# Optimization experiments

Measured on AMD Instinct MI355X. Metric: run time of the kernel, lower is better.

Reference implementation:

```python
import jax, jax.numpy as jnp
import numpy as np

D_MODEL = 1024
NUM_HEADS = 16
D_K = D_MODEL // NUM_HEADS


def setup_inputs() -> dict:
    key = jax.random.key(0)
    ks = jax.random.split(key, 11)
    s = 1.0 / np.sqrt(D_MODEL)
    return {
        "Q": jax.random.normal(ks[0], (2, 2048, D_MODEL), jnp.float32),
        "K": jax.random.normal(ks[1], (2, 2048, D_MODEL), jnp.float32),
        "V": jax.random.normal(ks[2], (2, 2048, D_MODEL), jnp.float32),
        "W_Q": jax.random.uniform(ks[3], (D_MODEL, D_MODEL), jnp.float32, -s, s),
        "b_Q": jax.random.uniform(ks[4], (D_MODEL,), jnp.float32, -s, s),
        "W_K": jax.random.uniform(ks[5], (D_K, D_MODEL), jnp.float32, -s, s),
        "b_K": jax.random.uniform(ks[6], (D_K,), jnp.float32, -s, s),
        "W_V": jax.random.uniform(ks[7], (D_K, D_MODEL), jnp.float32, -s, s),
        "b_V": jax.random.uniform(ks[8], (D_K,), jnp.float32, -s, s),
        "W_O": jax.random.uniform(ks[9], (D_MODEL, D_MODEL), jnp.float32, -s, s),
        "b_O": jax.random.uniform(ks[10], (D_MODEL,), jnp.float32, -s, s),
    }


def reference(Q, K, V, W_Q, b_Q, W_K, b_K, W_V, b_V, W_O, b_O):
    B, S, _ = Q.shape
    # Q projection -> [B, H, S, d_k]
    q = (Q @ W_Q.T + b_Q).reshape(B, S, NUM_HEADS, D_K).transpose(0, 2, 1, 3)
    # shared single-head K/V -> [B, S, d_k] (broadcast across heads)
    k = K @ W_K.T + b_K
    v = V @ W_V.T + b_V
    scale = 1.0 / jnp.sqrt(jnp.asarray(D_K, q.dtype))
    scores = jnp.einsum('bhqd,bkd->bhqk', q, k) * scale  # [B,H,S,S]
    attn = jax.nn.softmax(scores, axis=-1)
    out = jnp.einsum('bhqk,bkd->bhqd', attn, v)  # [B,H,S,d_k]
    out = out.transpose(0, 2, 1, 3).reshape(B, S, D_MODEL)
    return out @ W_O.T + b_O
```

## Files before the change

kernel.cpp:

```cpp
#include <hip/hip_runtime.h>
#include <hip/hip_bf16.h>
#include <math.h>

#define D_MODEL 1024
#define NUM_HEADS 16
#define DK 64
#define BATCH 2
#define SEQ 2048
#define MROWS (BATCH * SEQ)

#define QSCALE (0.125f * 1.4426950408889634f)

typedef __attribute__((ext_vector_type(8))) short bf16x8;
typedef __attribute__((ext_vector_type(4))) float f32x4;

static __device__ __forceinline__ short f2bf(float f) {
    __hip_bfloat16 h = __float2bfloat16(f);
    union { __hip_bfloat16 h; short s; } c; c.h = h; return c.s;
}

static __device__ __forceinline__ unsigned pkbf2(float a, float b) {
    __hip_bfloat162 h = __float22bfloat162_rn(make_float2(a, b));
    union { __hip_bfloat162 h; unsigned u; } c; c.h = h; return c.u;
}

static __device__ __forceinline__ void gload16(const void* g, void* l) {
    __builtin_amdgcn_global_load_lds(
        (const __attribute__((address_space(1))) unsigned int*)g,
        (__attribute__((address_space(3))) unsigned int*)l, 16, 0, 0);
}

__global__ __launch_bounds__(256) void cvt6(
    const float* __restrict__ q, const float* __restrict__ k,
    const float* __restrict__ v, const float* __restrict__ wq,
    const float* __restrict__ wo, const float* __restrict__ wk,
    const float* __restrict__ wv,
    short* __restrict__ qo, short* __restrict__ ko, short* __restrict__ vo,
    short* __restrict__ wqo, short* __restrict__ woo, short* __restrict__ wko,
    short* __restrict__ wvo)
{
    const int NB = (MROWS * D_MODEL) / 8;
    const int NW = (D_MODEL * D_MODEL) / 8;
    const int NS = (DK * D_MODEL) / 8;
    const int total = 3 * NB + 2 * NW + 2 * NS;
    for (int g = blockIdx.x * 256 + threadIdx.x; g < total; g += gridDim.x * 256) {
        const float* s; short* d; int x = g;
        if (x < NB)            { s = q;  d = qo;  }
        else if ((x -= NB) < NB) { s = k;  d = ko;  }
        else if ((x -= NB) < NB) { s = v;  d = vo;  }
        else if ((x -= NB) < NW) { s = wq; d = wqo; }
        else if ((x -= NW) < NW) { s = wo; d = woo; }
        else if ((x -= NW) < NS) { s = wk; d = wko; }
        else                     { x -= NS; s = wv; d = wvo; }
        float4 a = ((const float4*)s)[x * 2];
        float4 b = ((const float4*)s)[x * 2 + 1];
        uint4 hv;
        hv.x = pkbf2(a.x, a.y); hv.y = pkbf2(a.z, a.w);
        hv.z = pkbf2(b.x, b.y); hv.w = pkbf2(b.z, b.w);
        ((uint4*)d)[x] = hv;
    }
}

template<int MODE, int BM, int BN>
__global__ __launch_bounds__(256) void gemm97(
    const short* __restrict__ A, const short* __restrict__ W,
    const float* __restrict__ bias, void* __restrict__ Cp,
    const short* __restrict__ A2, const short* __restrict__ W2,
    const float* __restrict__ bias2, void* __restrict__ Cp2,
    int M, int N, int K, float outmult)
{
    constexpr int MI = BM / 32;
    constexpr int NI = BN / 32;
    constexpr int ACH = BM / 32;
    constexpr int WCH = BN / 32;
    __shared__ short As[BM * 64];
    __shared__ short Ws[BN * 64];

    int sel = 0;
    if (MODE == 2) {
        sel = blockIdx.y;
        if (sel) { A = A2; W = W2; bias = bias2; Cp = Cp2; }
    }
    const int bm = blockIdx.x * BM;
    const int bn = (MODE == 2) ? 0 : blockIdx.y * BN;
    const int tid = threadIdx.x;
    const int l = tid & 63, w = tid >> 6;
    const int lr = l & 15, lg = l >> 4;
    const int wm = (w >> 1) * (BM / 2), wn = (w & 1) * (BN / 2);

    f32x4 acc[MI][NI];
    #pragma unroll
    for (int mi = 0; mi < MI; mi++)
        #pragma unroll
        for (int ni = 0; ni < NI; ni++)
            acc[mi][ni] = (f32x4){0.f, 0.f, 0.f, 0.f};

    const int srow = l >> 3;
    const int scol = (l & 7) * 8;

    for (int k0 = 0; k0 < K; k0 += 64) {
        __syncthreads();
        #pragma unroll
        for (int i = 0; i < ACH; i++) {
            int c = w * ACH + i;
            gload16(A + (size_t)(bm + 8 * c + srow) * K + k0 + scol, As + c * 512);
        }
        #pragma unroll
        for (int i = 0; i < WCH; i++) {
            int c = w * WCH + i;
            gload16(W + (size_t)(bn + 8 * c + srow) * K + k0 + scol, Ws + c * 512);
        }
        __syncthreads();
        #pragma unroll
        for (int ks = 0; ks < 2; ks++) {
            bf16x8 af[MI], bf[NI];
            #pragma unroll
            for (int mi = 0; mi < MI; mi++)
                af[mi] = *(const bf16x8*)&As[(wm + mi * 16 + lr) * 64 + ks * 32 + 8 * lg];
            #pragma unroll
            for (int ni = 0; ni < NI; ni++)
                bf[ni] = *(const bf16x8*)&Ws[(wn + ni * 16 + lr) * 64 + ks * 32 + 8 * lg];
            #pragma unroll
            for (int mi = 0; mi < MI; mi++)
                #pragma unroll
                for (int ni = 0; ni < NI; ni++)
                    acc[mi][ni] = __builtin_amdgcn_mfma_f32_16x16x32_bf16(
                        af[mi], bf[ni], acc[mi][ni], 0, 0, 0);
        }
    }

    #pragma unroll
    for (int ni = 0; ni < NI; ni++) {
        int col = bn + wn + ni * 16 + lr;
        float bv = bias[col];
        #pragma unroll
        for (int mi = 0; mi < MI; mi++) {
            #pragma unroll
            for (int r = 0; r < 4; r++) {
                int row = bm + wm + mi * 16 + lg * 4 + r;
                float val = (acc[mi][ni][r] + bv) * outmult;
                if (MODE == 0) {
                    ((short*)Cp)[(size_t)row * N + col] = f2bf(val);
                } else if (MODE == 1) {
                    ((float*)Cp)[(size_t)row * N + col] = val;
                } else {
                    if (sel == 0) {
                        ((short*)Cp)[(size_t)row * DK + col] = f2bf(val);
                    } else {
                        int bi = row >> 11, si = row & (SEQ - 1);
                        int s6 = si & 63;
                        int sperm = (si & ~63) | (s6 & 32) |
                                    (((s6 >> 3) & 1) << 4) | (((s6 >> 2) & 1) << 3) |
                                    (((s6 >> 4) & 1) << 2) | (s6 & 3);
                        ((short*)Cp)[((size_t)bi * DK + col) * SEQ + sperm] = f2bf(val);
                    }
                }
            }
        }
    }
}

__global__ __launch_bounds__(256, 4) void mqa_attn_lds(
    const short* __restrict__ qb, const short* __restrict__ kb,
    const short* __restrict__ vt, short* __restrict__ ob)
{
    __shared__ char KsB[2][64 * 128];
    __shared__ char VsB[2][64 * 128];
    const int h = blockIdx.y, b = blockIdx.z;
    const int tid = threadIdx.x;
    const int l = tid & 63, w = tid >> 6;
    const int qg = w >> 1, kh = w & 1;
    const int lr = l & 15, lg = l >> 4;
    const int q0 = blockIdx.x * 64 + qg * 32;

    bf16x8 qf[2][2];
    #pragma unroll
    for (int qt = 0; qt < 2; qt++)
        #pragma unroll
        for (int kk = 0; kk < 2; kk++)
            qf[qt][kk] = *(const bf16x8*)(
                qb + (size_t)(b * SEQ + q0 + qt * 16 + lr) * D_MODEL + h * DK + kk * 32 + 8 * lg);

    int srow[2], scol[2];
    #pragma unroll
    for (int i = 0; i < 2; i++) {
        int s = i * 256 + w * 64 + l;
        srow[i] = s >> 3;
        int cb = (s & 7) * 16;
        scol[i] = (cb ^ ((srow[i] & 7) << 4)) >> 1;
    }

    f32x4 o[4][2];
    #pragma unroll
    for (int dt = 0; dt < 4; dt++)
        #pragma unroll
        for (int qt = 0; qt < 2; qt++)
            o[dt][qt] = (f32x4){0.f, 0.f, 0.f, 0.f};
    float l_l[2] = {0.f, 0.f};

    #pragma unroll
    for (int i = 0; i < 2; i++) {
        gload16(kb + (size_t)(b * SEQ + 0 + srow[i]) * DK + scol[i],
                KsB[0] + (i * 256 + w * 64) * 16);
        gload16(vt + (size_t)(b * DK + srow[i]) * SEQ + 0 + scol[i],
                VsB[0] + (i * 256 + w * 64) * 16);
    }

    for (int t = 0; t < SEQ / 64; t++) {
        const int cur = t & 1;
        const int kt = t * 64;
        __syncthreads();
        if (t + 1 < SEQ / 64) {
            const int ktn = kt + 64;
            #pragma unroll
            for (int i = 0; i < 2; i++) {
                gload16(kb + (size_t)(b * SEQ + ktn + srow[i]) * DK + scol[i],
                        KsB[cur ^ 1] + (i * 256 + w * 64) * 16);
                gload16(vt + (size_t)(b * DK + srow[i]) * SEQ + ktn + scol[i],
                        VsB[cur ^ 1] + (i * 256 + w * 64) * 16);
            }
        }
        const char* Kc = KsB[cur];
        const char* Vc = VsB[cur];

        f32x4 s[2][2];
        #pragma unroll
        for (int qt = 0; qt < 2; qt++)
            #pragma unroll
            for (int j = 0; j < 2; j++) s[qt][j] = (f32x4){0.f, 0.f, 0.f, 0.f};
        #pragma unroll
        for (int kk = 0; kk < 2; kk++) {
            bf16x8 kf[2];
            #pragma unroll
            for (int j = 0; j < 2; j++) {
                int row = kh * 32 + j * 16 + lr;
                kf[j] = *(const bf16x8*)(Kc + row * 128 + ((kk * 64 + 16 * lg) ^ ((row & 7) << 4)));
            }
            __builtin_amdgcn_s_setprio(1);
            #pragma unroll
            for (int qt = 0; qt < 2; qt++)
                #pragma unroll
                for (int j = 0; j < 2; j++)
                    s[qt][j] = __builtin_amdgcn_mfma_f32_16x16x32_bf16(
                        kf[j], qf[qt][kk], s[qt][j], 0, 0, 0);
            __builtin_amdgcn_s_setprio(0);
        }

        bf16x8 vf[4];
        #pragma unroll
        for (int dt = 0; dt < 4; dt++) {
            int row = dt * 16 + lr;
            vf[dt] = *(const bf16x8*)(Vc + row * 128 + ((kh * 64 + 16 * lg) ^ ((row & 7) << 4)));
        }

        union { unsigned u[4]; bf16x8 v; } pku[2];
        #pragma unroll
        for (int qt = 0; qt < 2; qt++) {
            float p[2][4];
            float rs = 0.f;
            #pragma unroll
            for (int j = 0; j < 2; j++) {
                p[j][0] = __builtin_amdgcn_exp2f(s[qt][j][0]);
                p[j][1] = __builtin_amdgcn_exp2f(s[qt][j][1]);
                p[j][2] = __builtin_amdgcn_exp2f(s[qt][j][2]);
                p[j][3] = __builtin_amdgcn_exp2f(s[qt][j][3]);
                rs += (p[j][0] + p[j][1]) + (p[j][2] + p[j][3]);
            }
            l_l[qt] += rs;
            pku[qt].u[0] = pkbf2(p[0][0], p[0][1]);
            pku[qt].u[1] = pkbf2(p[0][2], p[0][3]);
            pku[qt].u[2] = pkbf2(p[1][0], p[1][1]);
            pku[qt].u[3] = pkbf2(p[1][2], p[1][3]);
        }

        __builtin_amdgcn_s_setprio(1);
        #pragma unroll
        for (int dt = 0; dt < 4; dt++)
            #pragma unroll
            for (int qt = 0; qt < 2; qt++)
                o[dt][qt] = __builtin_amdgcn_mfma_f32_16x16x32_bf16(
                    vf[dt], pku[qt].v, o[dt][qt], 0, 0, 0);
        __builtin_amdgcn_s_setprio(0);
    }

    float lw[2];
    #pragma unroll
    for (int qt = 0; qt < 2; qt++) {
        float x = l_l[qt];
        x += __shfl_xor(x, 16);
        x += __shfl_xor(x, 32);
        lw[qt] = x;
    }
    __syncthreads();
    float* OS = (float*)KsB;
    float* ML = (float*)VsB;
    if (kh == 1) {
        #pragma unroll
        for (int dt = 0; dt < 4; dt++)
            #pragma unroll
            for (int qt = 0; qt < 2; qt++)
                #pragma unroll
                for (int r = 0; r < 4; r++)
                    OS[(dt * 8 + qt * 4 + r) * 128 + qg * 64 + l] = o[dt][qt][r];
        if (l < 16) {
            ML[(qg * 2 + 0) * 16 + l] = lw[0];
            ML[(qg * 2 + 1) * 16 + l] = lw[1];
        }
    }
    __syncthreads();
    if (kh == 0) {
        #pragma unroll
        for (int qt = 0; qt < 2; qt++) {
            float lt = lw[qt] + ML[(qg * 2 + qt) * 16 + lr];
            float inv = 1.0f / lt;
            size_t grow = (size_t)(b * SEQ + q0 + qt * 16 + lr);
            #pragma unroll
            for (int dt = 0; dt < 4; dt++) {
                float v0 = o[dt][qt][0] + OS[(dt * 8 + qt * 4 + 0) * 128 + qg * 64 + l];
                float v1 = o[dt][qt][1] + OS[(dt * 8 + qt * 4 + 1) * 128 + qg * 64 + l];
                float v2 = o[dt][qt][2] + OS[(dt * 8 + qt * 4 + 2) * 128 + qg * 64 + l];
                float v3 = o[dt][qt][3] + OS[(dt * 8 + qt * 4 + 3) * 128 + qg * 64 + l];
                uint2 pk;
                pk.x = pkbf2(v0 * inv, v1 * inv);
                pk.y = pkbf2(v2 * inv, v3 * inv);
                *(uint2*)(ob + grow * D_MODEL + h * DK + dt * 16 + lg * 4) = pk;
            }
        }
    }
}

extern "C" void kernel_launch(void* const* d_in, const int* in_sizes, int n_in,
                              void* d_out, int out_size, void* d_ws, size_t ws_size,
                              hipStream_t stream) {
    const float* Q   = (const float*)d_in[0];
    const float* K   = (const float*)d_in[1];
    const float* V   = (const float*)d_in[2];
    const float* W_Q = (const float*)d_in[3];
    const float* b_Q = (const float*)d_in[4];
    const float* W_K = (const float*)d_in[5];
    const float* b_K = (const float*)d_in[6];
    const float* W_V = (const float*)d_in[7];
    const float* b_V = (const float*)d_in[8];
    const float* W_O = (const float*)d_in[9];
    const float* b_O = (const float*)d_in[10];
    float* out = (float*)d_out;

    short* Qb  = (short*)d_ws;
    short* Kb  = Qb  + (size_t)MROWS * D_MODEL;
    short* Vb  = Kb  + (size_t)MROWS * D_MODEL;
    short* WQb = Vb  + (size_t)MROWS * D_MODEL;
    short* WKb = WQb + (size_t)D_MODEL * D_MODEL;
    short* WVb = WKb + (size_t)DK * D_MODEL;
    short* WOb = WVb + (size_t)DK * D_MODEL;
    short* qb  = WOb + (size_t)D_MODEL * D_MODEL;
    short* kb  = qb  + (size_t)MROWS * D_MODEL;
    short* vt  = kb  + (size_t)MROWS * DK;
    short* aws = vt  + (size_t)MROWS * DK;

    cvt6<<<2048, 256, 0, stream>>>(Q, K, V, W_Q, W_O, W_K, W_V,
                                   Qb, Kb, Vb, WQb, WOb, WKb, WVb);

    gemm97<0, 64, 128><<<dim3(MROWS / 64, D_MODEL / 128), 256, 0, stream>>>(
        Qb, WQb, b_Q, qb, nullptr, nullptr, nullptr, nullptr,
        MROWS, D_MODEL, D_MODEL, QSCALE);
    gemm97<2, 64, 64><<<dim3(MROWS / 64, 2), 256, 0, stream>>>(
        Kb, WKb, b_K, kb, Vb, WVb, b_V, vt, MROWS, DK, D_MODEL, 1.0f);
    mqa_attn_lds<<<dim3(SEQ / 64, NUM_HEADS, BATCH), 256, 0, stream>>>(
        qb, kb, vt, aws);
    gemm97<1, 64, 128><<<dim3(MROWS / 64, D_MODEL / 128), 256, 0, stream>>>(
        aws, WOb, b_O, out, nullptr, nullptr, nullptr, nullptr,
        MROWS, D_MODEL, D_MODEL, 1.0f);
}
```

Before: 120.4 us.

## Load K/V fragments directly from global memory instead of LDS staging

```diff
diff --git a/kernel.cpp b/kernel.cpp
--- a/kernel.cpp
+++ b/kernel.cpp
@@ -160,12 +160,12 @@
     }
 }
 
-__global__ __launch_bounds__(256, 4) void mqa_attn_lds(
+__global__ __launch_bounds__(256, 4) void mqa_attn_l2(
     const short* __restrict__ qb, const short* __restrict__ kb,
     const short* __restrict__ vt, short* __restrict__ ob)
 {
-    __shared__ char KsB[2][64 * 128];
-    __shared__ char VsB[2][64 * 128];
+    __shared__ float OS[32 * 128];
+    __shared__ float ML[4 * 16];
     const int h = blockIdx.y, b = blockIdx.z;
     const int tid = threadIdx.x;
     const int l = tid & 63, w = tid >> 6;
@@ -181,15 +181,6 @@
             qf[qt][kk] = *(const bf16x8*)(
                 qb + (size_t)(b * SEQ + q0 + qt * 16 + lr) * D_MODEL + h * DK + kk * 32 + 8 * lg);
 
-    int srow[2], scol[2];
-    #pragma unroll
-    for (int i = 0; i < 2; i++) {
-        int s = i * 256 + w * 64 + l;
-        srow[i] = s >> 3;
-        int cb = (s & 7) * 16;
-        scol[i] = (cb ^ ((srow[i] & 7) << 4)) >> 1;
-    }
-
     f32x4 o[4][2];
     #pragma unroll
     for (int dt = 0; dt < 4; dt++)
@@ -198,60 +189,40 @@
             o[dt][qt] = (f32x4){0.f, 0.f, 0.f, 0.f};
     float l_l[2] = {0.f, 0.f};
 
-    #pragma unroll
-    for (int i = 0; i < 2; i++) {
-        gload16(kb + (size_t)(b * SEQ + 0 + srow[i]) * DK + scol[i],
-                KsB[0] + (i * 256 + w * 64) * 16);
-        gload16(vt + (size_t)(b * DK + srow[i]) * SEQ + 0 + scol[i],
-                VsB[0] + (i * 256 + w * 64) * 16);
-    }
+    const short* Kb_ = kb + (size_t)b * SEQ * DK;
+    const short* Vb_ = vt + (size_t)b * DK * SEQ;
 
     for (int t = 0; t < SEQ / 64; t++) {
-        const int cur = t & 1;
         const int kt = t * 64;
-        __syncthreads();
-        if (t + 1 < SEQ / 64) {
-            const int ktn = kt + 64;
-            #pragma unroll
-            for (int i = 0; i < 2; i++) {
-                gload16(kb + (size_t)(b * SEQ + ktn + srow[i]) * DK + scol[i],
-                        KsB[cur ^ 1] + (i * 256 + w * 64) * 16);
-                gload16(vt + (size_t)(b * DK + srow[i]) * SEQ + ktn + scol[i],
-                        VsB[cur ^ 1] + (i * 256 + w * 64) * 16);
-            }
-        }
-        const char* Kc = KsB[cur];
-        const char* Vc = VsB[cur];
+
+        bf16x8 kf[2][2];
+        #pragma unroll
+        for (int kk = 0; kk < 2; kk++)
+            #pragma unroll
+            for (int j = 0; j < 2; j++)
+                kf[kk][j] = *(const bf16x8*)(
+                    Kb_ + (size_t)(kt + kh * 32 + j * 16 + lr) * DK + kk * 32 + 8 * lg);
+        bf16x8 vf[4];
+        #pragma unroll
+        for (int dt = 0; dt < 4; dt++)
+            vf[dt] = *(const bf16x8*)(
+                Vb_ + (size_t)(dt * 16 + lr) * SEQ + kt + kh * 32 + 8 * lg);
 
         f32x4 s[2][2];
         #pragma unroll
         for (int qt = 0; qt < 2; qt++)
             #pragma unroll
             for (int j = 0; j < 2; j++) s[qt][j] = (f32x4){0.f, 0.f, 0.f, 0.f};
-        #pragma unroll
-        for (int kk = 0; kk < 2; kk++) {
-            bf16x8 kf[2];
-            #pragma unroll
-            for (int j = 0; j < 2; j++) {
-                int row = kh * 32 + j * 16 + lr;
-                kf[j] = *(const bf16x8*)(Kc + row * 128 + ((kk * 64 + 16 * lg) ^ ((row & 7) << 4)));
-            }
-            __builtin_amdgcn_s_setprio(1);
+        __builtin_amdgcn_s_setprio(1);
+        #pragma unroll
+        for (int kk = 0; kk < 2; kk++)
             #pragma unroll
             for (int qt = 0; qt < 2; qt++)
                 #pragma unroll
                 for (int j = 0; j < 2; j++)
                     s[qt][j] = __builtin_amdgcn_mfma_f32_16x16x32_bf16(
-                        kf[j], qf[qt][kk], s[qt][j], 0, 0, 0);
-            __builtin_amdgcn_s_setprio(0);
-        }
-
-        bf16x8 vf[4];
-        #pragma unroll
-        for (int dt = 0; dt < 4; dt++) {
-            int row = dt * 16 + lr;
-            vf[dt] = *(const bf16x8*)(Vc + row * 128 + ((kh * 64 + 16 * lg) ^ ((row & 7) << 4)));
-        }
+                        kf[kk][j], qf[qt][kk], s[qt][j], 0, 0, 0);
+        __builtin_amdgcn_s_setprio(0);
 
         union { unsigned u[4]; bf16x8 v; } pku[2];
         #pragma unroll
@@ -291,9 +262,6 @@
         x += __shfl_xor(x, 32);
         lw[qt] = x;
     }
-    __syncthreads();
-    float* OS = (float*)KsB;
-    float* ML = (float*)VsB;
     if (kh == 1) {
         #pragma unroll
         for (int dt = 0; dt < 4; dt++)
@@ -365,7 +333,7 @@
         MROWS, D_MODEL, D_MODEL, QSCALE);
     gemm97<2, 64, 64><<<dim3(MROWS / 64, 2), 256, 0, stream>>>(
         Kb, WKb, b_K, kb, Vb, WVb, b_V, vt, MROWS, DK, D_MODEL, 1.0f);
-    mqa_attn_lds<<<dim3(SEQ / 64, NUM_HEADS, BATCH), 256, 0, stream>>>(
+    mqa_attn_l2<<<dim3(SEQ / 64, NUM_HEADS, BATCH), 256, 0, stream>>>(
         qb, kb, vt, aws);
     gemm97<1, 64, 128><<<dim3(MROWS / 64, D_MODEL / 128), 256, 0, stream>>>(
         aws, WOb, b_O, out, nullptr, nullptr, nullptr, nullptr,
```

New measurement: 191.7 us. 59.2% more time.

## Share K/V LDS tiles across two heads per attention block

Applied to the files above, without the earlier changes.

```diff
diff --git a/kernel.cpp b/kernel.cpp
--- a/kernel.cpp
+++ b/kernel.cpp
@@ -160,16 +160,18 @@
     }
 }
 
-__global__ __launch_bounds__(256, 4) void mqa_attn_lds(
+__global__ __launch_bounds__(512, 4) void mqa_attn_lds(
     const short* __restrict__ qb, const short* __restrict__ kb,
     const short* __restrict__ vt, short* __restrict__ ob)
 {
     __shared__ char KsB[2][64 * 128];
     __shared__ char VsB[2][64 * 128];
-    const int h = blockIdx.y, b = blockIdx.z;
+    __shared__ float ML[128];
+    const int b = blockIdx.z;
     const int tid = threadIdx.x;
     const int l = tid & 63, w = tid >> 6;
-    const int qg = w >> 1, kh = w & 1;
+    const int h2 = w >> 2, qg = (w >> 1) & 1, kh = w & 1;
+    const int hd = blockIdx.y * 2 + h2;
     const int lr = l & 15, lg = l >> 4;
     const int q0 = blockIdx.x * 64 + qg * 32;
 
@@ -179,16 +181,10 @@
         #pragma unroll
         for (int kk = 0; kk < 2; kk++)
             qf[qt][kk] = *(const bf16x8*)(
-                qb + (size_t)(b * SEQ + q0 + qt * 16 + lr) * D_MODEL + h * DK + kk * 32 + 8 * lg);
-
-    int srow[2], scol[2];
-    #pragma unroll
-    for (int i = 0; i < 2; i++) {
-        int s = i * 256 + w * 64 + l;
-        srow[i] = s >> 3;
-        int cb = (s & 7) * 16;
-        scol[i] = (cb ^ ((srow[i] & 7) << 4)) >> 1;
-    }
+                qb + (size_t)(b * SEQ + q0 + qt * 16 + lr) * D_MODEL + hd * DK + kk * 32 + 8 * lg);
+
+    const int srow = tid >> 3;
+    const int scol = (((tid & 7) * 16) ^ ((srow & 7) << 4)) >> 1;
 
     f32x4 o[4][2];
     #pragma unroll
@@ -198,13 +194,8 @@
             o[dt][qt] = (f32x4){0.f, 0.f, 0.f, 0.f};
     float l_l[2] = {0.f, 0.f};
 
-    #pragma unroll
-    for (int i = 0; i < 2; i++) {
-        gload16(kb + (size_t)(b * SEQ + 0 + srow[i]) * DK + scol[i],
-                KsB[0] + (i * 256 + w * 64) * 16);
-        gload16(vt + (size_t)(b * DK + srow[i]) * SEQ + 0 + scol[i],
-                VsB[0] + (i * 256 + w * 64) * 16);
-    }
+    gload16(kb + (size_t)(b * SEQ + 0 + srow) * DK + scol, KsB[0] + w * 64 * 16);
+    gload16(vt + (size_t)(b * DK + srow) * SEQ + 0 + scol, VsB[0] + w * 64 * 16);
 
     for (int t = 0; t < SEQ / 64; t++) {
         const int cur = t & 1;
@@ -212,13 +203,10 @@
         __syncthreads();
         if (t + 1 < SEQ / 64) {
             const int ktn = kt + 64;
-            #pragma unroll
-            for (int i = 0; i < 2; i++) {
-                gload16(kb + (size_t)(b * SEQ + ktn + srow[i]) * DK + scol[i],
-                        KsB[cur ^ 1] + (i * 256 + w * 64) * 16);
-                gload16(vt + (size_t)(b * DK + srow[i]) * SEQ + ktn + scol[i],
-                        VsB[cur ^ 1] + (i * 256 + w * 64) * 16);
-            }
+            gload16(kb + (size_t)(b * SEQ + ktn + srow) * DK + scol,
+                    KsB[cur ^ 1] + w * 64 * 16);
+            gload16(vt + (size_t)(b * DK + srow) * SEQ + ktn + scol,
+                    VsB[cur ^ 1] + w * 64 * 16);
         }
         const char* Kc = KsB[cur];
         const char* Vc = VsB[cur];
@@ -292,8 +280,7 @@
         lw[qt] = x;
     }
     __syncthreads();
-    float* OS = (float*)KsB;
-    float* ML = (float*)VsB;
+    float* OS = h2 ? (float*)VsB : (float*)KsB;
     if (kh == 1) {
         #pragma unroll
         for (int dt = 0; dt < 4; dt++)
@@ -303,15 +290,15 @@
                 for (int r = 0; r < 4; r++)
                     OS[(dt * 8 + qt * 4 + r) * 128 + qg * 64 + l] = o[dt][qt][r];
         if (l < 16) {
-            ML[(qg * 2 + 0) * 16 + l] = lw[0];
-            ML[(qg * 2 + 1) * 16 + l] = lw[1];
+            ML[((h2 * 2 + qg) * 2 + 0) * 16 + l] = lw[0];
+            ML[((h2 * 2 + qg) * 2 + 1) * 16 + l] = lw[1];
         }
     }
     __syncthreads();
     if (kh == 0) {
         #pragma unroll
         for (int qt = 0; qt < 2; qt++) {
-            float lt = lw[qt] + ML[(qg * 2 + qt) * 16 + lr];
+            float lt = lw[qt] + ML[((h2 * 2 + qg) * 2 + qt) * 16 + lr];
             float inv = 1.0f / lt;
             size_t grow = (size_t)(b * SEQ + q0 + qt * 16 + lr);
             #pragma unroll
@@ -323,7 +310,7 @@
                 uint2 pk;
                 pk.x = pkbf2(v0 * inv, v1 * inv);
                 pk.y = pkbf2(v2 * inv, v3 * inv);
-                *(uint2*)(ob + grow * D_MODEL + h * DK + dt * 16 + lg * 4) = pk;
+                *(uint2*)(ob + grow * D_MODEL + hd * DK + dt * 16 + lg * 4) = pk;
             }
         }
     }
@@ -365,7 +352,7 @@
         MROWS, D_MODEL, D_MODEL, QSCALE);
     gemm97<2, 64, 64><<<dim3(MROWS / 64, 2), 256, 0, stream>>>(
         Kb, WKb, b_K, kb, Vb, WVb, b_V, vt, MROWS, DK, D_MODEL, 1.0f);
-    mqa_attn_lds<<<dim3(SEQ / 64, NUM_HEADS, BATCH), 256, 0, stream>>>(
+    mqa_attn_lds<<<dim3(SEQ / 64, NUM_HEADS / 2, BATCH), 512, 0, stream>>>(
         qb, kb, vt, aws);
     gemm97<1, 64, 128><<<dim3(MROWS / 64, D_MODEL / 128), 256, 0, stream>>>(
         aws, WOb, b_O, out, nullptr, nullptr, nullptr, nullptr,
```

New measurement: 116.2 us. 3.5% less time.
